# Optimization experiments

Measured on AMD Instinct MI355X. Metric: run time of the kernel, lower is better.

## Reference

```python
import jax, jax.numpy as jnp
import numpy as np
import math

D_MODEL = 2048
Q_HEAD = 32
KV_HEAD = 8
HEAD_DIM = D_MODEL // Q_HEAD  # 64
GROUP = Q_HEAD // KV_HEAD     # 4
B, T = 2, 2048


def setup_inputs() -> dict:
    key = jax.random.key(0)
    ks = jax.random.split(key, 9)
    s = 0.02
    return {
        "x": jax.random.normal(ks[0], (B, T, D_MODEL), dtype=jnp.float32),
        "Wq": jax.random.normal(ks[1], (D_MODEL, Q_HEAD * HEAD_DIM), dtype=jnp.float32) * s,
        "bq": jnp.zeros((Q_HEAD * HEAD_DIM,), dtype=jnp.float32),
        "Wk": jax.random.normal(ks[2], (D_MODEL, KV_HEAD * HEAD_DIM), dtype=jnp.float32) * s,
        "bk": jnp.zeros((KV_HEAD * HEAD_DIM,), dtype=jnp.float32),
        "Wv": jax.random.normal(ks[3], (D_MODEL, KV_HEAD * HEAD_DIM), dtype=jnp.float32) * s,
        "bv": jnp.zeros((KV_HEAD * HEAD_DIM,), dtype=jnp.float32),
        "Wo": jax.random.normal(ks[4], (D_MODEL, D_MODEL), dtype=jnp.float32) * s,
        "bo": jnp.zeros((D_MODEL,), dtype=jnp.float32),
    }


def reference(x, Wq, bq, Wk, bk, Wv, bv, Wo, bo):
    Bx, Tx, C = x.shape
    # projections -> [B, H, T, Dh]
    q = (x @ Wq + bq).reshape(Bx, Tx, Q_HEAD, HEAD_DIM).transpose(0, 2, 1, 3)
    k = (x @ Wk + bk).reshape(Bx, Tx, KV_HEAD, HEAD_DIM).transpose(0, 2, 1, 3)
    v = (x @ Wv + bv).reshape(Bx, Tx, KV_HEAD, HEAD_DIM).transpose(0, 2, 1, 3)
    # GQA: repeat each KV head `GROUP` times (repeat_interleave semantics)
    k = jnp.repeat(k, GROUP, axis=1)
    v = jnp.repeat(v, GROUP, axis=1)
    score = jnp.einsum("bhqd,bhkd->bhqk", q, k) / math.sqrt(HEAD_DIM)
    causal = jnp.tril(jnp.ones((Tx, Tx), dtype=bool))
    score = jnp.where(causal, score, -jnp.inf)
    attn = jax.nn.softmax(score, axis=-1)
    out = jnp.einsum("bhqk,bhkd->bhqd", attn, v)
    out = out.transpose(0, 2, 1, 3).reshape(Bx, Tx, C)
    return out @ Wo + bo
```

## Files before the change

kernel.cpp:

```cpp
#include <hip/hip_runtime.h>
#include <hip/hip_bf16.h>

typedef unsigned short u16;
typedef __attribute__((ext_vector_type(8)))  __bf16 bf16x8;
typedef __attribute__((ext_vector_type(8)))  unsigned short u16x8;
typedef __attribute__((ext_vector_type(4)))  unsigned short u16x4;
typedef __attribute__((ext_vector_type(4)))  float f32x4;
typedef __attribute__((ext_vector_type(16))) float f32x16;
typedef __attribute__((ext_vector_type(4)))  unsigned u32x4;

#define MFMA(a, b, c)   __builtin_amdgcn_mfma_f32_16x16x32_bf16((a), (b), (c), 0, 0, 0)
#define MFMA32(a, b, c) __builtin_amdgcn_mfma_f32_32x32x16_bf16((a), (b), (c), 0, 0, 0)

__device__ __forceinline__ u16 f2b(float f) {
  union { float f; unsigned u; } x; x.f = f;
  unsigned r = x.u + 0x7fffu + ((x.u >> 16) & 1u);
  return (u16)(r >> 16);
}

__device__ __forceinline__ unsigned pack2(float lo, float hi) {
  const __bf16 a = (__bf16)lo, b = (__bf16)hi;
  return (unsigned)__builtin_bit_cast(u16, a) | ((unsigned)__builtin_bit_cast(u16, b) << 16);
}

__device__ __forceinline__ bf16x8 ld2x64(const u16* p) {
  union { u16x4 h[2]; bf16x8 v; } u;
  u.h[0] = *(const u16x4*)p;
  u.h[1] = *(const u16x4*)(p + 4);
  return u.v;
}

__device__ __forceinline__ void gl_lds16(void* lds, const void* g) {
  __builtin_amdgcn_global_load_lds(
      (const __attribute__((address_space(1))) void*)g,
      (__attribute__((address_space(3))) void*)lds, 16, 0, 0);
}

__global__ __launch_bounds__(256) void cvt_fused_kernel(
    const float* __restrict__ x, u16* __restrict__ xb,
    const float* __restrict__ Wq, const float* __restrict__ Wk,
    const float* __restrict__ Wv, const float* __restrict__ Wo,
    u16* __restrict__ Wqt, u16* __restrict__ Wkt,
    u16* __restrict__ Wvt, u16* __restrict__ Wot) {
  __shared__ u16 t[32][36];
  if (blockIdx.x < 8192) {
    const int i = (blockIdx.x * 256 + threadIdx.x) * 4;
    f32x4 v = *(const f32x4*)(x + i);
    u16x4 o;
    o[0] = f2b(v[0]); o[1] = f2b(v[1]); o[2] = f2b(v[2]); o[3] = f2b(v[3]);
    *(u16x4*)(xb + i) = o;
    return;
  }
  const int bx = blockIdx.x - 8192;
  const int xw = bx >> 6;
  const int k0 = (bx & 63) * 32;
  const float* W; u16* Wt; int N, n0;
  if (xw < 64)      { W = Wq; Wt = Wqt; N = 2048; n0 = xw * 32; }
  else if (xw < 80) { W = Wk; Wt = Wkt; N = 512;  n0 = (xw - 64) * 32; }
  else if (xw < 96) { W = Wv; Wt = Wvt; N = 512;  n0 = (xw - 80) * 32; }
  else              { W = Wo; Wt = Wot; N = 2048; n0 = (xw - 96) * 32; }
  const int r = threadIdx.x >> 3, c4 = (threadIdx.x & 7) * 4;
  f32x4 v = *(const f32x4*)&W[(size_t)(k0 + r) * N + n0 + c4];
  t[c4 + 0][r] = f2b(v[0]);
  t[c4 + 1][r] = f2b(v[1]);
  t[c4 + 2][r] = f2b(v[2]);
  t[c4 + 3][r] = f2b(v[3]);
  __syncthreads();
  u16x4 o;
  o[0] = t[r][c4]; o[1] = t[r][c4 + 1]; o[2] = t[r][c4 + 2]; o[3] = t[r][c4 + 3];
  *(u16x4*)&Wt[(size_t)(n0 + r) * 2048 + k0 + c4] = o;
}

template <bool OUT_BF16>
__device__ __forceinline__ void gemm_body(const u16* __restrict__ A, const u16* __restrict__ Bt,
                                          const float* __restrict__ bias, void* __restrict__ C,
                                          const int N, const int n0, const int m0, const float scale) {
  __shared__ __align__(16) u16 As[128 * 32];
  __shared__ __align__(16) u16 Bs[128 * 32];
  const int tid = threadIdx.x;
  const int lane = tid & 63, wv = tid >> 6;
  const int l15 = lane & 15, lg = lane >> 4;
  const int wm = wv >> 2, wn = wv & 3;
  const int srow = tid >> 2;
  const int g = tid & 3;
  const int gs = g ^ ((srow >> 1) & 3);

  f32x4 acc[4][2] = {};

  for (int k0 = 0; k0 < 2048; k0 += 32) {
    gl_lds16(&As[wv << 9], A  + (((size_t)(m0 + srow)) << 11) + k0 + gs * 8);
    gl_lds16(&Bs[wv << 9], Bt + (((size_t)(n0 + srow)) << 11) + k0 + gs * 8);
    __syncthreads();
    bf16x8 af[4], bfr[2];
#pragma unroll
    for (int t = 0; t < 4; t++) {
      const int ra = wm * 64 + t * 16 + l15;
      af[t] = *(const bf16x8*)&As[ra * 32 + ((lg ^ ((ra >> 1) & 3)) << 3)];
    }
#pragma unroll
    for (int u = 0; u < 2; u++) {
      const int rb = wn * 32 + u * 16 + l15;
      bfr[u] = *(const bf16x8*)&Bs[rb * 32 + ((lg ^ ((rb >> 1) & 3)) << 3)];
    }
#pragma unroll
    for (int mt = 0; mt < 4; mt++)
#pragma unroll
      for (int nt = 0; nt < 2; nt++)
        acc[mt][nt] = MFMA(af[mt], bfr[nt], acc[mt][nt]);
    __syncthreads();
  }

#pragma unroll
  for (int nt = 0; nt < 2; nt++) {
    const int col = n0 + wn * 32 + nt * 16 + l15;
    const float bc = bias[col];
#pragma unroll
    for (int mt = 0; mt < 4; mt++) {
#pragma unroll
      for (int r = 0; r < 4; r++) {
        const int row = m0 + wm * 64 + mt * 16 + lg * 4 + r;
        const float v = (acc[mt][nt][r] + bc) * scale;
        if (OUT_BF16) ((u16*)C)[(size_t)row * N + col] = f2b(v);
        else          ((float*)C)[(size_t)row * N + col] = v;
      }
    }
  }
}

__global__ __launch_bounds__(512, 6) void qkv_gemm_kernel(
    const u16* __restrict__ xb,
    const u16* __restrict__ Wqt, const u16* __restrict__ Wkt, const u16* __restrict__ Wvt,
    const float* __restrict__ bq, const float* __restrict__ bk, const float* __restrict__ bv,
    u16* __restrict__ Qb, u16* __restrict__ Kb, u16* __restrict__ Vb) {
  const int nb = blockIdx.x;
  const u16* Bt; const float* bias; u16* out; int N, n0; float scale;
  if (nb < 16)      { Bt = Wqt; bias = bq; out = Qb; N = 2048; n0 = nb * 128;        scale = 0.125f * 1.44269504f; }
  else if (nb < 20) { Bt = Wkt; bias = bk; out = Kb; N = 512;  n0 = (nb - 16) * 128; scale = 1.0f; }
  else              { Bt = Wvt; bias = bv; out = Vb; N = 512;  n0 = (nb - 20) * 128; scale = 1.0f; }
  gemm_body<true>(xb, Bt, bias, out, N, n0, blockIdx.y * 128, scale);
}

__global__ __launch_bounds__(512, 6) void oproj_kernel(const u16* __restrict__ Ab,
                                                       const u16* __restrict__ Wot,
                                                       const float* __restrict__ bo,
                                                       float* __restrict__ out) {
  gemm_body<false>(Ab, Wot, bo, out, 2048, blockIdx.x * 128, blockIdx.y * 128, 1.0f);
}

__global__ __launch_bounds__(512, 4) void attn_kernel(const u16* __restrict__ Qb,
                                                      const u16* __restrict__ Kb,
                                                      const u16* __restrict__ Vb,
                                                      u16* __restrict__ Ab) {
  const int i = blockIdx.x;
  const int j = i & 255;
  const int kh = j & 7, b = (j >> 3) & 1;
  const int p16 = j >> 4;
  const int qt = (i < 256) ? (31 - p16) : p16;

  const int tid = threadIdx.x;
  const int lane = tid & 63, wv = tid >> 6;
  const int hh = wv & 3, qh = wv >> 2;
  const int h = kh * 4 + hh;
  const int l31 = lane & 31, hi = lane >> 5;
  const int swz = (l31 & 7) << 3;

  __shared__ __align__(16) u16 Ks[2][64 * 64];
  __shared__ __align__(16) u16 Vt[2][64 * 68];

  const int skv = tid >> 3;
  const int sc8 = tid & 7;
  const int sd0 = sc8 * 8;

  const u16* Kbase = Kb + (size_t)(b * 2048) * 512 + kh * 64;
  const u16* Vbase = Vb + (size_t)(b * 2048) * 512 + kh * 64;

  const int q0 = qt * 64;

  bf16x8 qf[4];
  {
    const u16* qp = Qb + (size_t)(b * 2048 + q0 + qh * 32 + l31) * 2048 + h * 64 + hi * 8;
#pragma unroll
    for (int c = 0; c < 4; c++) qf[c] = *(const bf16x8*)(qp + c * 16);
  }
  f32x16 ot[2] = {};
  float mrow = -30000.0f, srow = 0.f;

  int cur = 0;
  {
    gl_lds16(&Ks[0][wv << 9], Kbase + ((size_t)skv << 9) + ((sc8 ^ (skv & 7)) << 3));
    u16x8 vr = *(const u16x8*)(Vbase + ((size_t)skv << 9) + sd0);
#pragma unroll
    for (int j8 = 0; j8 < 8; j8++) {
      const int jj = (j8 + sc8) & 7;
      const int d = sd0 + jj;
      Vt[0][d * 68 + skv] = vr[jj];
    }
  }
  for (int it = 0; it <= qt; ++it) {
    __syncthreads();
    const bool pre = (it < qt);
    u16x8 vnx;
    if (pre) {
      const size_t roff = (size_t)((it + 1) * 64 + skv) << 9;
      gl_lds16(&Ks[cur ^ 1][wv << 9], Kbase + roff + ((sc8 ^ (skv & 7)) << 3));
      vnx = *(const u16x8*)(Vbase + roff + sd0);
    }
    const u16* Kc = Ks[cur];
    const u16* Vc = Vt[cur];

    f32x16 sc2[2] = {};
#pragma unroll
    for (int c = 0; c < 4; c++) {
      const int dblk = (c * 16 + hi * 8) ^ swz;
#pragma unroll
      for (int kvh = 0; kvh < 2; kvh++) {
        bf16x8 kf = *(const bf16x8*)&Kc[(kvh * 32 + l31) * 64 + dblk];
        sc2[kvh] = MFMA32(kf, qf[c], sc2[kvh]);
      }
    }
    if (it == qt) {
      const int q = qh * 32 + l31;
#pragma unroll
      for (int kvh = 0; kvh < 2; kvh++)
#pragma unroll
        for (int r = 0; r < 16; r++) {
          const int kv = kvh * 32 + (r & 3) + 8 * (r >> 2) + 4 * hi;
          if (kv > q) sc2[kvh][r] = -30000.0f;
        }
    }
    float tm = fmaxf(sc2[0][0], sc2[0][1]);
#pragma unroll
    for (int kvh = 0; kvh < 2; kvh++)
#pragma unroll
      for (int r = (kvh ? 0 : 2); r < 16; r++) tm = fmaxf(tm, sc2[kvh][r]);
    tm = fmaxf(tm, __shfl_xor(tm, 32));
    if (__any(tm > mrow + 8.0f)) {
      const float mnew = fmaxf(mrow, tm);
      const float scl = __builtin_amdgcn_exp2f(mrow - mnew);
      mrow = mnew;
      srow *= scl;
#pragma unroll
      for (int dh = 0; dh < 2; dh++)
#pragma unroll
        for (int r = 0; r < 16; r++) ot[dh][r] *= scl;
    }
    float ps = 0.f;
#pragma unroll
    for (int kvh = 0; kvh < 2; kvh++) {
      unsigned pk[8];
#pragma unroll
      for (int j8 = 0; j8 < 8; j8++) {
        const float p0 = __builtin_amdgcn_exp2f(sc2[kvh][2 * j8] - mrow);
        const float p1 = __builtin_amdgcn_exp2f(sc2[kvh][2 * j8 + 1] - mrow);
        ps += p0 + p1;
        pk[j8] = pack2(p0, p1);
      }
#pragma unroll
      for (int tt = 0; tt < 2; tt++) {
        const int t = kvh * 2 + tt;
        const unsigned a0 = pk[4 * tt + 0], a1 = pk[4 * tt + 1];
        const unsigned b0 = pk[4 * tt + 2], b1 = pk[4 * tt + 3];
        const unsigned s0 = hi ? a0 : b0, s1 = hi ? a1 : b1;
        const unsigned r0 = (unsigned)__shfl_xor((int)s0, 32);
        const unsigned r1 = (unsigned)__shfl_xor((int)s1, 32);
        u32x4 pw;
        pw[0] = hi ? r0 : a0;
        pw[1] = hi ? r1 : a1;
        pw[2] = hi ? b0 : r0;
        pw[3] = hi ? b1 : r1;
        const bf16x8 pf = __builtin_bit_cast(bf16x8, pw);
#pragma unroll
        for (int dh = 0; dh < 2; dh++) {
          bf16x8 vf = ld2x64(&Vc[(dh * 32 + l31) * 68 + t * 16 + hi * 8]);
          ot[dh] = MFMA32(vf, pf, ot[dh]);
        }
      }
    }
    ps += __shfl_xor(ps, 32);
    srow += ps;
    if (pre) {
#pragma unroll
      for (int j8 = 0; j8 < 8; j8++) {
        const int jj = (j8 + sc8) & 7;
        const int d = sd0 + jj;
        Vt[cur ^ 1][d * 68 + skv] = vnx[jj];
      }
    }
    cur ^= 1;
  }
  __syncthreads();
  u16* Sx = (wv < 4) ? &Ks[0][0] + wv * 2048 : &Vt[0][0] + (wv - 4) * 2048;
  const float inv = 1.0f / srow;
#pragma unroll
  for (int dh = 0; dh < 2; dh++)
#pragma unroll
    for (int jr = 0; jr < 8; jr++) {
      const unsigned w = pack2(ot[dh][2 * jr] * inv, ot[dh][2 * jr + 1] * inv);
      const int d = dh * 32 + 8 * (jr >> 1) + (jr & 1) * 2 + 4 * hi;
      *(unsigned*)&Sx[l31 * 64 + (d ^ swz)] = w;
    }
  __syncthreads();
#pragma unroll
  for (int rep = 0; rep < 4; rep++) {
    const int chunk = rep * 64 + lane;
    const int qr = chunk >> 3, cc = chunk & 7;
    u16x8 val = *(const u16x8*)&Sx[qr * 64 + ((cc * 8) ^ ((qr & 7) << 3))];
    *(u16x8*)&Ab[(size_t)(b * 2048 + q0 + qh * 32 + qr) * 2048 + h * 64 + cc * 8] = val;
  }
}

extern "C" void kernel_launch(void* const* d_in, const int* in_sizes, int n_in,
                              void* d_out, int out_size, void* d_ws, size_t ws_size,
                              hipStream_t stream) {
  const float* x  = (const float*)d_in[0];
  const float* Wq = (const float*)d_in[1];
  const float* bq = (const float*)d_in[2];
  const float* Wk = (const float*)d_in[3];
  const float* bk = (const float*)d_in[4];
  const float* Wv = (const float*)d_in[5];
  const float* bv = (const float*)d_in[6];
  const float* Wo = (const float*)d_in[7];
  const float* bo = (const float*)d_in[8];

  char* ws = (char*)d_ws;
  u16* xb  = (u16*)(ws + 0);
  u16* Ab  = (u16*)(ws + 0);
  u16* Qb  = (u16*)(ws + 16777216);
  u16* Kb  = (u16*)(ws + 33554432);
  u16* Vb  = (u16*)(ws + 37748736);
  u16* Wqt = (u16*)(ws + 41943040);
  u16* Wkt = (u16*)(ws + 50331648);
  u16* Wvt = (u16*)(ws + 52428800);
  u16* Wot = (u16*)(ws + 54525952);

  cvt_fused_kernel<<<dim3(8192 + 160 * 64), 256, 0, stream>>>(
      x, xb, Wq, Wk, Wv, Wo, Wqt, Wkt, Wvt, Wot);

  qkv_gemm_kernel<<<dim3(24, 32), 512, 0, stream>>>(xb, Wqt, Wkt, Wvt, bq, bk, bv, Qb, Kb, Vb);
  attn_kernel<<<dim3(512), 512, 0, stream>>>(Qb, Kb, Vb, Ab);
  oproj_kernel<<<dim3(16, 32), 512, 0, stream>>>(Ab, Wot, bo, (float*)d_out);
}
```

Before: 211.4 us.

## Split long causal attention tiles across two KV halves and merge partials

```diff
diff --git a/kernel.cpp b/kernel.cpp
--- a/kernel.cpp
+++ b/kernel.cpp
@@ -16,6 +16,10 @@
   union { float f; unsigned u; } x; x.f = f;
   unsigned r = x.u + 0x7fffu + ((x.u >> 16) & 1u);
   return (u16)(r >> 16);
+}
+
+__device__ __forceinline__ float b2f(u16 v) {
+  return __builtin_bit_cast(float, ((unsigned)v) << 16);
 }
 
 __device__ __forceinline__ unsigned pack2(float lo, float hi) {
@@ -147,15 +151,42 @@
   gemm_body<false>(Ab, Wot, bo, out, 2048, blockIdx.x * 128, blockIdx.y * 128, 1.0f);
 }
 
+static __device__ const unsigned char kOrder[43] = {
+  84, 83, 82, 81, 80,
+  62, 63, 60,
+  79,
+  61, 58, 59, 56,
+  78,
+  57, 54, 55, 52,
+  77,
+  53, 50, 51, 48,
+  76,
+  49, 46, 47, 44,
+  75,
+  45, 42, 43,
+  74,
+  73, 72, 71, 70, 69, 68, 67, 66, 65, 64
+};
+
 __global__ __launch_bounds__(512, 4) void attn_kernel(const u16* __restrict__ Qb,
                                                       const u16* __restrict__ Kb,
                                                       const u16* __restrict__ Vb,
-                                                      u16* __restrict__ Ab) {
-  const int i = blockIdx.x;
-  const int j = i & 255;
-  const int kh = j & 7, b = (j >> 3) & 1;
-  const int p16 = j >> 4;
-  const int qt = (i < 256) ? (31 - p16) : p16;
+                                                      u16* __restrict__ Ab,
+                                                      u16* __restrict__ Opart,
+                                                      float* __restrict__ msBuf) {
+  const int e = kOrder[blockIdx.x >> 4];
+  const int combo = blockIdx.x & 15;
+  const int kh = combo & 7, b = combo >> 3;
+  int qt, kvlo, kvhi, chk;
+  if (e >= 64) { qt = e - 64; kvlo = 0; kvhi = qt + 1; chk = -1; }
+  else {
+    qt = e >> 1;
+    const int half = e & 1;
+    const int mid = (qt + 2) >> 1;
+    kvlo = half ? mid : 0;
+    kvhi = half ? qt + 1 : mid;
+    chk = (combo * 11 + (qt - 21)) * 2 + half;
+  }
 
   const int tid = threadIdx.x;
   const int lane = tid & 63, wv = tid >> 6;
@@ -187,8 +218,8 @@
 
   int cur = 0;
   {
-    gl_lds16(&Ks[0][wv << 9], Kbase + ((size_t)skv << 9) + ((sc8 ^ (skv & 7)) << 3));
-    u16x8 vr = *(const u16x8*)(Vbase + ((size_t)skv << 9) + sd0);
+    gl_lds16(&Ks[0][wv << 9], Kbase + (((size_t)(kvlo * 64 + skv)) << 9) + ((sc8 ^ (skv & 7)) << 3));
+    u16x8 vr = *(const u16x8*)(Vbase + (((size_t)(kvlo * 64 + skv)) << 9) + sd0);
 #pragma unroll
     for (int j8 = 0; j8 < 8; j8++) {
       const int jj = (j8 + sc8) & 7;
@@ -196,9 +227,9 @@
       Vt[0][d * 68 + skv] = vr[jj];
     }
   }
-  for (int it = 0; it <= qt; ++it) {
+  for (int it = kvlo; it < kvhi; ++it) {
     __syncthreads();
-    const bool pre = (it < qt);
+    const bool pre = (it + 1 < kvhi);
     u16x8 vnx;
     if (pre) {
       const size_t roff = (size_t)((it + 1) * 64 + skv) << 9;
@@ -288,6 +319,11 @@
     }
     cur ^= 1;
   }
+  if (chk >= 0 && hi == 0) {
+    const int msb = ((chk * 4 + hh) * 64 + qh * 32 + l31) * 2;
+    msBuf[msb] = mrow;
+    msBuf[msb + 1] = srow;
+  }
   __syncthreads();
   u16* Sx = (wv < 4) ? &Ks[0][0] + wv * 2048 : &Vt[0][0] + (wv - 4) * 2048;
   const float inv = 1.0f / srow;
@@ -302,10 +338,39 @@
   __syncthreads();
 #pragma unroll
   for (int rep = 0; rep < 4; rep++) {
-    const int chunk = rep * 64 + lane;
-    const int qr = chunk >> 3, cc = chunk & 7;
+    const int u = rep * 64 + lane;
+    const int qr = u >> 3, cc = u & 7;
     u16x8 val = *(const u16x8*)&Sx[qr * 64 + ((cc * 8) ^ ((qr & 7) << 3))];
-    *(u16x8*)&Ab[(size_t)(b * 2048 + q0 + qh * 32 + qr) * 2048 + h * 64 + cc * 8] = val;
+    if (chk < 0)
+      *(u16x8*)&Ab[(size_t)(b * 2048 + q0 + qh * 32 + qr) * 2048 + h * 64 + cc * 8] = val;
+    else
+      *(u16x8*)&Opart[(size_t)((chk * 4 + hh) * 64 + qh * 32 + qr) * 64 + cc * 8] = val;
+  }
+}
+
+__global__ __launch_bounds__(256) void merge_kernel(const u16* __restrict__ Opart,
+                                                    const float* __restrict__ msBuf,
+                                                    u16* __restrict__ Ab) {
+  const int sp = blockIdx.x, h = blockIdx.y;
+  const int combo = sp / 11, qt = 21 + sp % 11;
+  const int kh = combo & 7, b = combo >> 3;
+  const int c0 = (sp * 2) * 4 + h, c1 = (sp * 2 + 1) * 4 + h;
+#pragma unroll
+  for (int u = threadIdx.x; u < 512; u += 256) {
+    const int q = u >> 3, dc = u & 7;
+    const float m1 = msBuf[(c0 * 64 + q) * 2], s1 = msBuf[(c0 * 64 + q) * 2 + 1];
+    const float m2 = msBuf[(c1 * 64 + q) * 2], s2 = msBuf[(c1 * 64 + q) * 2 + 1];
+    const float m = fmaxf(m1, m2);
+    const float w1 = s1 * __builtin_amdgcn_exp2f(m1 - m);
+    const float w2 = s2 * __builtin_amdgcn_exp2f(m2 - m);
+    const float inv = 1.0f / (w1 + w2);
+    u16x8 o1 = *(const u16x8*)&Opart[(size_t)(c0 * 64 + q) * 64 + dc * 8];
+    u16x8 o2 = *(const u16x8*)&Opart[(size_t)(c1 * 64 + q) * 64 + dc * 8];
+    u16x8 out;
+#pragma unroll
+    for (int jj = 0; jj < 8; jj++)
+      out[jj] = f2b((b2f(o1[jj]) * w1 + b2f(o2[jj]) * w2) * inv);
+    *(u16x8*)&Ab[(size_t)(b * 2048 + qt * 64 + q) * 2048 + (kh * 4 + h) * 64 + dc * 8] = out;
   }
 }
 
@@ -332,11 +397,14 @@
   u16* Wkt = (u16*)(ws + 50331648);
   u16* Wvt = (u16*)(ws + 52428800);
   u16* Wot = (u16*)(ws + 54525952);
+  u16*   Opart = (u16*)(ws + 41943040);
+  float* msBuf = (float*)(ws + 41943040 + 11534336);
 
   cvt_fused_kernel<<<dim3(8192 + 160 * 64), 256, 0, stream>>>(
       x, xb, Wq, Wk, Wv, Wo, Wqt, Wkt, Wvt, Wot);
 
   qkv_gemm_kernel<<<dim3(24, 32), 512, 0, stream>>>(xb, Wqt, Wkt, Wvt, bq, bk, bv, Qb, Kb, Vb);
-  attn_kernel<<<dim3(512), 512, 0, stream>>>(Qb, Kb, Vb, Ab);
+  attn_kernel<<<dim3(16 * 43), 512, 0, stream>>>(Qb, Kb, Vb, Ab, Opart, msBuf);
+  merge_kernel<<<dim3(176, 4), 256, 0, stream>>>(Opart, msBuf, Ab);
   oproj_kernel<<<dim3(16, 32), 512, 0, stream>>>(Ab, Wot, bo, (float*)d_out);
 }
```

Result: no change. 208.7 us (-1.3%).
